# Kernel tuning notes

Hardware: AMD Instinct MI355X
Metric: run time of the kernel (lower is better)

Reference implementation:

```python
import jax, jax.numpy as jnp
import numpy as np

B, S, E, H, D, F = 8, 512, 768, 12, 64, 3072
EPS = 1e-5
SQRT3 = np.float32(np.sqrt(3.0))


def _ln(x, g, b):
    m = jnp.mean(x, -1, keepdims=True)
    v = jnp.mean((x - m) ** 2, -1, keepdims=True)
    return (x - m) * jax.lax.rsqrt(v + EPS) * g + b


def _gelu_new(x):
    return 0.5 * x * (1.0 + jnp.tanh(0.7978845608028654 * (x + 0.044715 * x * x * x)))


def _heads(t):  # [B,T,E] -> [B,T,H,D]
    return t.reshape(t.shape[0], t.shape[1], H, D)


def _self_attn(xl, Wq, Wk, Wv, Wo, bo, mask):
    q = _heads(xl @ Wq)
    k = _heads(xl @ Wk)
    v = _heads(xl @ Wv)
    w = jnp.einsum('bqhd,bkhd->bhqk', q, k) / 8.0  # scale=True, sqrt(64)
    w = jnp.where(mask, -1e9, w)
    p = jax.nn.softmax(w, axis=-1)
    o = jnp.einsum('bhqk,bkhd->bqhd', p, v).reshape(xl.shape)
    present = jnp.stack([k.transpose(0, 2, 1, 3), v.transpose(0, 2, 1, 3)])  # [2,B,H,S,D]
    return o @ Wo + bo, present


def _cross_attn(xl, el, wq, bq, wk, bk, wv, bv, wp, bp, mask):
    q = _heads(xl @ wq + bq)
    k = _heads(el @ wk + bk)
    v = _heads(el @ wv + bv)
    w = jnp.einsum('bqhd,bkhd->bhqk', q, k) / 8.0
    w = jnp.where(mask, -1e4, w)
    p = jax.nn.softmax(w, axis=-1)
    o = jnp.einsum('bhqk,bkhd->bqhd', p, v).reshape(xl.shape)
    return o @ wp + bp  # Conv1D: x @ W + b


def _block(x, encoder_output, mask_queries, mask_sa, mask_enc, tau,
           Wq, Wk, Wv, Wo, bo,
           fcq_w, fcq_b, fck_w, fck_b, fcv_w, fcv_b, cproj_w, cproj_b,
           ln1_g, ln1_b, ln2_g, ln2_b,
           cfc_w, cfc_b, cproj2_w, cproj2_b,
           a1_w, a1_b, a2_w, a2_b, a3_w, a3_b):
    thr = jnp.asarray(tau, jnp.float32)
    sa, present = _self_attn(_ln(x, ln1_g, ln1_b), Wq, Wk, Wv, Wo, bo, mask_sa)
    a = x + sa  # resid dropout = identity (eval)
    al = _ln(a, ln1_g, ln1_b)

    def cross(idx):
        el = _ln(encoder_output[:, idx], ln1_g, ln1_b)
        return _cross_attn(al, el, fcq_w, fcq_b, fck_w, fck_b, fcv_w, fcv_b,
                           cproj_w, cproj_b, mask_enc)

    e1, e2, e3 = cross(0), cross(1), cross(2)

    def gate(e, w, b):
        alpha = jax.nn.sigmoid(jnp.concatenate([a, e], -1) @ w + b)
        lm = jnp.where(alpha > thr, 1.0, 0.0)
        vm = jnp.where(alpha < 1.0 - thr, 1.0, 0.0)
        return alpha * lm * a + (1.0 - alpha) * vm * e

    enc_att = (gate(e1, a1_w, a1_b) + gate(e2, a2_w, a2_b) + gate(e3, a3_w, a3_b)) / SQRT3
    aq = enc_att * mask_queries
    m = _gelu_new(_ln(aq, ln2_g, ln2_b) @ cfc_w + cfc_b) @ cproj2_w + cproj2_b
    out = (aq + m) * mask_queries
    return out, present


def setup_inputs() -> dict:
    key = jax.random.key(0)
    ks = jax.random.split(key, 40)
    p = lambda k, shp: (jax.random.normal(k, shp, jnp.float32) * 0.02)
    x = jax.random.normal(ks[0], (B, S, E), jnp.float32)
    encoder_output = jax.random.normal(ks[1], (B, 3, S, E), jnp.float32)
    mask_queries = jnp.ones((B, S, 1), jnp.float32)
    causal = ~jnp.tril(jnp.ones((S, S), bool))  # True = masked
    mask_self_attention = jnp.broadcast_to(causal[None, None], (B, 1, S, S))
    mask_encoder = jax.random.bernoulli(ks[2], 0.1, (B, 1, 1, S))
    d = dict(x=x, encoder_output=encoder_output, mask_queries=mask_queries,
             mask_self_attention=mask_self_attention, mask_encoder=mask_encoder,
             i=0, tau=0,
             Wq=p(ks[3], (E, E)), Wk=p(ks[4], (E, E)), Wv=p(ks[5], (E, E)),
             Wo=p(ks[6], (E, E)), bo=jnp.zeros((E,), jnp.float32),
             fcq_w=p(ks[7], (E, E)), fcq_b=jnp.zeros((E,), jnp.float32),
             fck_w=p(ks[8], (E, E)), fck_b=jnp.zeros((E,), jnp.float32),
             fcv_w=p(ks[9], (E, E)), fcv_b=jnp.zeros((E,), jnp.float32),
             cproj_w=p(ks[10], (E, E)), cproj_b=jnp.zeros((E,), jnp.float32),
             ln1_g=jnp.ones((E,), jnp.float32), ln1_b=jnp.zeros((E,), jnp.float32),
             ln2_g=jnp.ones((E,), jnp.float32), ln2_b=jnp.zeros((E,), jnp.float32),
             cfc_w=p(ks[11], (E, F)), cfc_b=jnp.zeros((F,), jnp.float32),
             cproj2_w=p(ks[12], (F, E)), cproj2_b=jnp.zeros((E,), jnp.float32),
             a1_w=p(ks[13], (2 * E, E)), a1_b=jnp.zeros((E,), jnp.float32),
             a2_w=p(ks[14], (2 * E, E)), a2_b=jnp.zeros((E,), jnp.float32),
             a3_w=p(ks[15], (2 * E, E)), a3_b=jnp.zeros((E,), jnp.float32))
    return d


def reference(x, encoder_output, mask_queries, mask_self_attention, mask_encoder, i, tau,
              Wq, Wk, Wv, Wo, bo,
              fcq_w, fcq_b, fck_w, fck_b, fcv_w, fcv_b, cproj_w, cproj_b,
              ln1_g, ln1_b, ln2_g, ln2_b,
              cfc_w, cfc_b, cproj2_w, cproj2_b,
              a1_w, a1_b, a2_w, a2_b, a3_w, a3_b):
    return _block(x, encoder_output, mask_queries, mask_self_attention, mask_encoder, tau,
                  Wq, Wk, Wv, Wo, bo,
                  fcq_w, fcq_b, fck_w, fck_b, fcv_w, fcv_b, cproj_w, cproj_b,
                  ln1_g, ln1_b, ln2_g, ln2_b,
                  cfc_w, cfc_b, cproj2_w, cproj2_b,
                  a1_w, a1_b, a2_w, a2_b, a3_w, a3_b)
```

## Files before the change

### kernel.cpp

```cpp
#include <hip/hip_runtime.h>
#include <hip/hip_bf16.h>
#include <math.h>

typedef __hip_bfloat16 bf16;
typedef __attribute__((ext_vector_type(8))) short s16x8;
typedef __attribute__((ext_vector_type(4))) float f32x4;

#define BB 8
#define SS 512
#define EE 768
#define HH 12
#define DD 64
#define FF 3072
#define NTOK (BB * SS)
#define NE ((size_t)NTOK * EE)

#define TM 128
#define TN 128
#define TK 32

#define QT 64
#define KT 64

#define FLAG_RES  4
#define FLAG_GELU 8
#define FLAG_FIN  16
#define FLAG_CBSD 32
#define FLAG_QKV  128
#define FLAG_KV   256
#define FLAG_GSEG 512

#define AS1 const __attribute__((address_space(1))) void*
#define AS3 __attribute__((address_space(3))) void*

__device__ __forceinline__ float gelu_new(float x) {
    float u2 = 1.5957691216057308f * (x + 0.044715f * x * x * x);
    return x / (1.0f + __expf(-u2));
}

__global__ __launch_bounds__(256) void tcast_all_kernel(
    const float* s0, const float* s1, const float* s2, const float* s3,
    const float* s4, const float* s5, const float* s6, const float* s7,
    const float* s8, const float* s9, const float* s10, const float* s11,
    const float* s12,
    bf16* d0, bf16* d1, bf16* d2, bf16* d3, bf16* d4, bf16* d5, bf16* d6,
    bf16* d7, bf16* d8, bf16* d9, bf16* d10, bf16* d11, bf16* d12,
    const float* fckb, const float* fcvb, const float* a0, const float* a1,
    const float* a2, float* kvb, float* gb)
{
    int bid = blockIdx.x;
    int tid = threadIdx.x;
    if (bid >= 12672) {
        int i = (bid - 12672) * 256 + tid;
        int seg = i / 768, off = i % 768;
        if (seg == 0)      kvb[off]       = fckb[off];
        else if (seg == 1) kvb[768 + off] = fcvb[off];
        else if (seg == 2) gb[off]        = a0[off];
        else if (seg == 3) gb[768 + off]  = a1[off];
        else               gb[1536 + off] = a2[off];
        return;
    }
    const int start[14] = {0, 576, 1152, 1728, 2304, 2880, 3456, 4032,
                           4608, 5760, 6912, 8064, 10368, 12672};
    const float* srcs[13] = {s0,s1,s2,s3,s4,s5,s6,s7,s8,s9,s10,s11,s12};
    bf16* dsts[13] = {d0,d1,d2,d3,d4,d5,d6,d7,d8,d9,d10,d11,d12};

    int idx = 0;
    #pragma unroll
    for (int i = 1; i < 13; ++i) if (bid >= start[i]) idx = i;
    int R = (idx < 8) ? 768 : (idx < 11) ? 1536 : (idx == 11) ? 768 : 3072;
    int C = (idx < 8) ? 768 : (idx < 11) ? 768 : (idx == 11) ? 3072 : 768;
    const float* src = srcs[idx];
    bf16* dst = dsts[idx];

    int t = bid - start[idx];
    int gx = C >> 5;
    int c0 = (t % gx) << 5;
    int r0 = (t / gx) << 5;

    __shared__ float tb[32][33];
    int x = tid & 31, y = tid >> 5;
    #pragma unroll
    for (int i = 0; i < 4; ++i) {
        int r = y + i * 8;
        tb[r][x] = src[(size_t)(r0 + r) * C + c0 + x];
    }
    __syncthreads();
    #pragma unroll
    for (int i = 0; i < 4; ++i) {
        int c = y + i * 8;
        dst[(size_t)(c0 + c) * R + r0 + x] = __float2bfloat16(tb[x][c]);
    }
}

__device__ __forceinline__ void ln_body(
    const float* __restrict__ x, bf16* __restrict__ y,
    const float* __restrict__ g, const float* __restrict__ bta, int tid)
{
    float v0 = x[tid], v1 = x[tid + 256], v2 = x[tid + 512];
    float s1 = v0 + v1 + v2;
    float s2 = v0 * v0 + v1 * v1 + v2 * v2;
    #pragma unroll
    for (int o = 32; o > 0; o >>= 1) {
        s1 += __shfl_down(s1, o);
        s2 += __shfl_down(s2, o);
    }
    __shared__ float r1[4], r2[4];
    if ((tid & 63) == 0) { r1[tid >> 6] = s1; r2[tid >> 6] = s2; }
    __syncthreads();
    float mean = (r1[0] + r1[1] + r1[2] + r1[3]) * (1.0f / 768.0f);
    float ssq  = (r2[0] + r2[1] + r2[2] + r2[3]) * (1.0f / 768.0f);
    float rstd = rsqrtf(ssq - mean * mean + 1e-5f);
    y[tid]       = __float2bfloat16((v0 - mean) * rstd * g[tid]       + bta[tid]);
    y[tid + 256] = __float2bfloat16((v1 - mean) * rstd * g[tid + 256] + bta[tid + 256]);
    y[tid + 512] = __float2bfloat16((v2 - mean) * rstd * g[tid + 512] + bta[tid + 512]);
}

__global__ __launch_bounds__(256) void ln_kernel(
    const float* __restrict__ in, bf16* __restrict__ out,
    const float* __restrict__ g, const float* __restrict__ bta)
{
    int row = blockIdx.x;
    ln_body(in + (size_t)row * EE, out + (size_t)row * EE, g, bta, threadIdx.x);
}

__global__ __launch_bounds__(256) void ln_all_kernel(
    const float* __restrict__ x, const float* __restrict__ enc,
    bf16* __restrict__ outx, bf16* __restrict__ outenc,
    const float* __restrict__ g, const float* __restrict__ bta)
{
    int row = blockIdx.x;
    if (row < NTOK) {
        ln_body(x + (size_t)row * EE, outx + (size_t)row * EE, g, bta, threadIdx.x);
    } else {
        int r = row - NTOK;
        int idx = r >> 12, b = (r >> 9) & 7, s = r & 511;
        ln_body(enc + (((size_t)b * 3 + idx) * SS + s) * EE,
                outenc + (size_t)r * EE, g, bta, threadIdx.x);
    }
}

template <int FLAGS>
__device__ __forceinline__ void mgemm_body(
    int bx, int by, bf16* smem,
    const bf16* __restrict__ A, const bf16* __restrict__ A2,
    const bf16* __restrict__ Wt, const float* __restrict__ bias,
    float* __restrict__ Cf, bf16* __restrict__ Cb, bf16* __restrict__ Cb2,
    int ldcb, const float* __restrict__ Rsrc, const float* __restrict__ maskq,
    int Nn, int K, int lda)
{
    constexpr bool f_res  = FLAGS & FLAG_RES;
    constexpr bool f_gelu = FLAGS & FLAG_GELU;
    constexpr bool f_fin  = FLAGS & FLAG_FIN;
    constexpr bool f_cbsd = FLAGS & FLAG_CBSD;
    constexpr bool f_qkv  = FLAGS & FLAG_QKV;
    constexpr bool f_kv   = FLAGS & FLAG_KV;
    constexpr bool f_gseg = FLAGS & FLAG_GSEG;

    const int BUFE = TM * TK + TN * TK;
    int tid = threadIdx.x;
    int w = tid >> 6, l = tid & 63;
    int row0 = bx * TM, col0 = by * TN;

    int wr = (w >> 1) * 64, wc = (w & 1) * 64;
    int lr = l & 15, lg = l >> 4;

    const bf16* Wb = Wt;
    const float* bb_ = bias;
    if constexpr (f_gseg) {
        int seg = row0 >> 12;
        Wb = Wt + (size_t)seg * 1536 * 768;
        bb_ = bias + seg * 768;
    }

    f32x4 acc[4][4];
    #pragma unroll
    for (int m = 0; m < 4; ++m)
        #pragma unroll
        for (int n = 0; n < 4; ++n) acc[m][n] = (f32x4){0.f, 0.f, 0.f, 0.f};

    auto stage = [&](int buf, int kb) {
        bf16* As_ = smem + buf * BUFE;
        bf16* Bs_ = As_ + TM * TK;
        #pragma unroll
        for (int i = 0; i < 2; ++i) {
            int e = (i * 256 + tid) * 8;
            int r = e >> 5;
            int c = (e & 31) ^ ((r & 3) << 3);
            const bf16* asrc;
            if constexpr (f_gseg) {
                int kg = kb + c;
                if (kg < 768) asrc = A  + (size_t)((row0 + r) & 4095) * lda + kg;
                else          asrc = A2 + (size_t)(row0 + r) * lda + (kg - 768);
            } else {
                asrc = A + (size_t)(row0 + r) * lda + kb + c;
            }
            __builtin_amdgcn_global_load_lds((AS1)asrc,
                (AS3)((char*)As_ + i * 4096 + w * 1024), 16, 0, 0);
            __builtin_amdgcn_global_load_lds((AS1)(Wb + (size_t)(col0 + r) * K + kb + c),
                (AS3)((char*)Bs_ + i * 4096 + w * 1024), 16, 0, 0);
        }
    };

    int nk = K / TK;
    stage(0, 0);
    stage(1, TK);
    stage(2, 2 * TK);

    for (int t = 0; t < nk; ++t) {
        int cur = t % 3;
        int ahead = nk - 1 - t; if (ahead > 2) ahead = 2;
        if (ahead == 2)      asm volatile("s_waitcnt vmcnt(8)" ::: "memory");
        else if (ahead == 1) asm volatile("s_waitcnt vmcnt(4)" ::: "memory");
        else                 asm volatile("s_waitcnt vmcnt(0)" ::: "memory");
        __builtin_amdgcn_s_barrier();

        const char* As = (const char*)(smem + cur * BUFE);
        const char* Bs = As + TM * TK * 2;
        s16x8 af[4], bfr[4];
        #pragma unroll
        for (int m = 0; m < 4; ++m) {
            int row = wr + m * 16 + lr;
            af[m] = *(const s16x8*)(As + row * 64 +
                      ((lg * 16) ^ ((row & 3) << 4)));
        }
        #pragma unroll
        for (int n = 0; n < 4; ++n) {
            int row = wc + n * 16 + lr;
            bfr[n] = *(const s16x8*)(Bs + row * 64 +
                      ((lg * 16) ^ ((row & 3) << 4)));
        }
        #pragma unroll
        for (int m = 0; m < 4; ++m)
            #pragma unroll
            for (int n = 0; n < 4; ++n)
                acc[m][n] = __builtin_amdgcn_mfma_f32_16x16x32_bf16(
                    af[m], bfr[n], acc[m][n], 0, 0, 0);

        asm volatile("s_waitcnt lgkmcnt(0)" ::: "memory");
        __builtin_amdgcn_s_barrier();
        if (t + 3 < nk) stage(cur, (t + 3) * TK);
    }

    int gh0 = (col0 + wc) >> 6;

    if constexpr (f_qkv || f_kv || f_cbsd) {
        bool vquad = (f_qkv && gh0 >= 24) || (f_kv && gh0 >= 12);
        bf16* Tb = smem + w * 4096;
        int bb = (row0 + wr) >> 9;
        int s0 = (row0 + wr) & 511;

        #pragma unroll
        for (int m = 0; m < 4; ++m)
            #pragma unroll
            for (int n = 0; n < 4; ++n)
                #pragma unroll
                for (int j = 0; j < 4; ++j) {
                    int col = col0 + wc + n * 16 + lr;
                    float v = acc[m][n][j];
                    if (bb_) v += bb_[col];
                    int rl = m * 16 + lg * 4 + j, cl = n * 16 + lr;
                    if (vquad)
                        *(bf16*)((char*)Tb + cl * 128 + ((rl * 2) ^ ((cl & 7) << 4))) =
                            __float2bfloat16(v);
                    else
                        Tb[rl * 64 + (cl ^ ((rl & 7) << 3))] = __float2bfloat16(v);
                }
        if (vquad) {
            int hV = gh0 - (f_qkv ? 24 : 12);
            bf16* vb = Cb2 + (((size_t)bb * HH + hV) * DD) * SS + s0;
            #pragma unroll
            for (int p = 0; p < 8; ++p) {
                int dl = p * 8 + (l >> 3);
                int ch = l & 7;
                int cs = ch ^ (dl & 7);
                s16x8 vv = *(const s16x8*)((char*)Tb + dl * 128 + cs * 16);
                *(s16x8*)(vb + (size_t)dl * SS + ch * 8) = vv;
            }
            if constexpr (f_qkv) {
                asm volatile("s_waitcnt lgkmcnt(0)" ::: "memory");
                #pragma unroll
                for (int m = 0; m < 4; ++m)
                    #pragma unroll
                    for (int n = 0; n < 4; ++n)
                        #pragma unroll
                        for (int j = 0; j < 4; ++j) {
                            int rl = m * 16 + lg * 4 + j, cl = n * 16 + lr;
                            Tb[rl * 64 + (cl ^ ((rl & 7) << 3))] =
                                __float2bfloat16(acc[m][n][j]);
                        }
                bf16* vbhsd = (bf16*)Cf;
                bf16* dst2 = vbhsd + (((size_t)bb * HH + hV) * SS + s0) * DD;
                #pragma unroll
                for (int p = 0; p < 8; ++p) {
                    int rl = p * 8 + (l >> 3);
                    int c8 = (l & 7) * 8;
                    s16x8 vv = *(const s16x8*)&Tb[rl * 64 + (c8 ^ ((rl & 7) << 3))];
                    *(s16x8*)(dst2 + (size_t)rl * DD + c8) = vv;
                }
            }
        } else {
            bf16* dst;
            if constexpr (f_qkv)
                dst = (gh0 < 12)
                    ? Cb + (((size_t)bb * HH + gh0) * SS + s0) * DD
                    : Cb + NE + (((size_t)bb * HH + (gh0 - 12)) * SS + s0) * DD;
            else
                dst = Cb + (((size_t)bb * HH + gh0) * SS + s0) * DD;
            #pragma unroll
            for (int p = 0; p < 8; ++p) {
                int rl = p * 8 + (l >> 3);
                int c8 = (l & 7) * 8;
                s16x8 vv = *(const s16x8*)&Tb[rl * 64 + (c8 ^ ((rl & 7) << 3))];
                *(s16x8*)(dst + (size_t)rl * DD + c8) = vv;
            }
        }
    } else {
        #pragma unroll
        for (int m = 0; m < 4; ++m) {
            #pragma unroll
            for (int n = 0; n < 4; ++n) {
                #pragma unroll
                for (int j = 0; j < 4; ++j) {
                    int row = row0 + wr + m * 16 + lg * 4 + j;
                    int col = col0 + wc + n * 16 + lr;
                    size_t lin = (size_t)row * Nn + col;
                    float v = acc[m][n][j];
                    if (bb_)                 v += bb_[col];
                    if constexpr (f_res)     v += Rsrc[lin];
                    if constexpr (f_gelu)    v = gelu_new(v);
                    if constexpr (f_fin)     v = (Rsrc[lin] + v) * maskq[row];
                    if (Cf) Cf[lin] = v;
                    if (Cb) Cb[(size_t)row * ldcb + col] = __float2bfloat16(v);
                }
            }
        }
    }
}

template <int FLAGS>
__global__ __launch_bounds__(256) void mgemm_kernel(
    const bf16* __restrict__ A, const bf16* __restrict__ A2,
    const bf16* __restrict__ Wt, const float* __restrict__ bias,
    float* __restrict__ Cf, bf16* __restrict__ Cb, bf16* __restrict__ Cb2,
    int ldcb, const float* __restrict__ Rsrc, const float* __restrict__ maskq,
    int Nn, int K, int lda)
{
    __shared__ __align__(16) bf16 smem[3 * (TM * TK + TN * TK)];
    mgemm_body<FLAGS>(blockIdx.x, blockIdx.y, smem, A, A2, Wt, bias,
                      Cf, Cb, Cb2, ldcb, Rsrc, maskq, Nn, K, lda);
}

__global__ __launch_bounds__(256) void qkvkv_kernel(
    const bf16* __restrict__ lnb, const bf16* __restrict__ lnenc,
    const bf16* __restrict__ WqkvT, const bf16* __restrict__ fckvT,
    const float* __restrict__ kvb,
    bf16* __restrict__ vbhsd, bf16* __restrict__ qbhb, bf16* __restrict__ vbhb,
    bf16* __restrict__ kb_c, bf16* __restrict__ vb_c)
{
    __shared__ __align__(16) bf16 smem[3 * (TM * TK + TN * TK)];
    int bid = blockIdx.x;
    if (bid < 576) {
        mgemm_body<FLAG_QKV>(bid & 31, bid >> 5, smem, lnb, nullptr, WqkvT, nullptr,
                             (float*)vbhsd, qbhb, vbhb, 0, nullptr, nullptr, 2304, 768, 768);
    } else {
        int t = bid - 576;
        mgemm_body<FLAG_KV>(t % 96, t / 96, smem, lnenc, nullptr, fckvT, kvb,
                            nullptr, kb_c, vb_c, 0, nullptr, nullptr, 1536, 768, 768);
    }
}

__device__ __forceinline__ void fattn_body(
    int bh, int qt, bf16* sm,
    const bf16* __restrict__ Qb, const bf16* __restrict__ Kb,
    const bf16* __restrict__ Vb, const int* __restrict__ maskE,
    bf16* __restrict__ Out, int causal)
{
    int bp = bh / HH, h = bh % HH;
    int bq = bp & 7;
    int tid = threadIdx.x;
    int w = tid >> 6, l = tid & 63;
    int lr = l & 15, g = l >> 4;

    bf16* Qs = sm;
    bf16* Ks = sm + 4096;
    bf16* Vs = sm + 8192;
    bf16* Ps = sm + 12288;

    int p0 = w * 1024 + l * 16;
    {
        const char* qg = (const char*)(Qb + (((size_t)bq * HH + h) * SS + qt * QT) * DD);
        #pragma unroll
        for (int i = 0; i < 2; ++i) {
            int p = i * 4096 + p0;
            int row = p >> 7, cb = p & 127;
            int scb = cb ^ ((row & 7) << 4);
            __builtin_amdgcn_global_load_lds((AS1)(qg + row * 128 + scb),
                (AS3)((char*)Qs + i * 4096 + w * 1024), 16, 0, 0);
        }
    }

    float mrun[4], lrun[4];
    f32x4 oacc[4];
    #pragma unroll
    for (int j = 0; j < 4; ++j) { mrun[j] = -3.0e38f; lrun[j] = 0.f; }
    #pragma unroll
    for (int n = 0; n < 4; ++n) oacc[n] = (f32x4){0.f, 0.f, 0.f, 0.f};

    int ntiles = causal ? (qt + 1) : (SS / KT);
    int qrow_base = w * 16;

    for (int kt = 0; kt < ntiles; ++kt) {
        const char* kg = (const char*)(Kb + ((size_t)bh * SS + kt * KT) * DD);
        const char* vg = (const char*)(Vb + (size_t)bh * DD * SS + (size_t)kt * KT);
        #pragma unroll
        for (int i = 0; i < 2; ++i) {
            int p = i * 4096 + p0;
            int row = p >> 7, cb = p & 127;
            int scb = cb ^ ((row & 7) << 4);
            __builtin_amdgcn_global_load_lds((AS1)(kg + row * 128 + scb),
                (AS3)((char*)Ks + i * 4096 + w * 1024), 16, 0, 0);
            __builtin_amdgcn_global_load_lds((AS1)(vg + (size_t)row * (SS * 2) + scb),
                (AS3)((char*)Vs + i * 4096 + w * 1024), 16, 0, 0);
        }
        int km[4];
        if (maskE) {
            #pragma unroll
            for (int n = 0; n < 4; ++n)
                km[n] = maskE[(size_t)bq * SS + kt * KT + n * 16 + lr];
        }
        __syncthreads();

        f32x4 sacc[4];
        #pragma unroll
        for (int n = 0; n < 4; ++n) sacc[n] = (f32x4){0.f, 0.f, 0.f, 0.f};
        #pragma unroll
        for (int ks = 0; ks < 2; ++ks) {
            int qrow = qrow_base + lr;
            s16x8 aq = *(const s16x8*)((const char*)Qs +
                        qrow * 128 + ((ks * 64 + g * 16) ^ ((qrow & 7) << 4)));
            #pragma unroll
            for (int n = 0; n < 4; ++n) {
                int krow = n * 16 + lr;
                s16x8 bk = *(const s16x8*)((const char*)Ks +
                            krow * 128 + ((ks * 64 + g * 16) ^ ((krow & 7) << 4)));
                sacc[n] = __builtin_amdgcn_mfma_f32_16x16x32_bf16(aq, bk, sacc[n], 0, 0, 0);
            }
        }

        #pragma unroll
        for (int n = 0; n < 4; ++n) {
            #pragma unroll
            for (int j = 0; j < 4; ++j) {
                float v = sacc[n][j] * 0.125f;
                if (causal) {
                    if (kt == qt && (n * 16 + lr > qrow_base + 4 * g + j)) v = -3.0e38f;
                } else {
                    if (km[n] != 0) v = -1e4f;
                }
                sacc[n][j] = v;
            }
        }

        float mx[4];
        #pragma unroll
        for (int j = 0; j < 4; ++j)
            mx[j] = fmaxf(fmaxf(sacc[0][j], sacc[1][j]), fmaxf(sacc[2][j], sacc[3][j]));
        #pragma unroll
        for (int msk = 1; msk < 16; msk <<= 1) {
            #pragma unroll
            for (int j = 0; j < 4; ++j) mx[j] = fmaxf(mx[j], __shfl_xor(mx[j], msk));
        }
        float rs[4], psum[4];
        #pragma unroll
        for (int j = 0; j < 4; ++j) {
            float mn = fmaxf(mrun[j], mx[j]);
            rs[j] = __expf(mrun[j] - mn);
            mrun[j] = mn;
            psum[j] = 0.f;
        }
        #pragma unroll
        for (int n = 0; n < 4; ++n) {
            #pragma unroll
            for (int j = 0; j < 4; ++j) {
                float p = __expf(sacc[n][j] - mrun[j]);
                psum[j] += p;
                int prow = qrow_base + 4 * g + j;
                int key = n * 16 + lr;
                *(bf16*)((char*)Ps + prow * 128 + ((2 * key) ^ ((prow & 7) << 4))) =
                    __float2bfloat16(p);
            }
        }
        #pragma unroll
        for (int msk = 1; msk < 16; msk <<= 1) {
            #pragma unroll
            for (int j = 0; j < 4; ++j) psum[j] += __shfl_xor(psum[j], msk);
        }
        #pragma unroll
        for (int j = 0; j < 4; ++j) lrun[j] = lrun[j] * rs[j] + psum[j];
        #pragma unroll
        for (int n = 0; n < 4; ++n) {
            #pragma unroll
            for (int j = 0; j < 4; ++j) oacc[n][j] *= rs[j];
        }

        #pragma unroll
        for (int ks = 0; ks < 2; ++ks) {
            int prow = qrow_base + lr;
            s16x8 ap = *(const s16x8*)((const char*)Ps +
                        prow * 128 + ((ks * 64 + g * 16) ^ ((prow & 7) << 4)));
            #pragma unroll
            for (int n = 0; n < 4; ++n) {
                int vrow = n * 16 + lr;
                s16x8 bv = *(const s16x8*)((const char*)Vs +
                            vrow * 128 + ((ks * 64 + g * 16) ^ ((vrow & 7) << 4)));
                oacc[n] = __builtin_amdgcn_mfma_f32_16x16x32_bf16(ap, bv, oacc[n], 0, 0, 0);
            }
        }
        __syncthreads();
    }

    float inv[4];
    #pragma unroll
    for (int j = 0; j < 4; ++j) inv[j] = 1.0f / lrun[j];
    #pragma unroll
    for (int n = 0; n < 4; ++n) {
        #pragma unroll
        for (int j = 0; j < 4; ++j) {
            int q = qt * QT + qrow_base + 4 * g + j;
            int d = n * 16 + lr;
            Out[((size_t)bp * SS + q) * EE + h * DD + d] =
                __float2bfloat16(oacc[n][j] * inv[j]);
        }
    }
}

__global__ __launch_bounds__(256) void fattn2_kernel(
    const bf16* __restrict__ Qb, const bf16* __restrict__ Kb,
    const bf16* __restrict__ Vb, const int* __restrict__ maskE,
    bf16* __restrict__ Out, int causal)
{
    __shared__ __align__(16) bf16 sm[4 * 4096];
    fattn_body(blockIdx.x, blockIdx.y, sm, Qb, Kb, Vb, maskE, Out, causal);
}

__global__ __launch_bounds__(256) void fattn_self_cast_kernel(
    const bf16* __restrict__ Qb, const bf16* __restrict__ Kb,
    const bf16* __restrict__ Vb, bf16* __restrict__ Out,
    const bf16* __restrict__ kb, const bf16* __restrict__ vb,
    float* __restrict__ kp, float* __restrict__ vp)
{
    __shared__ __align__(16) bf16 sm[4 * 4096];
    int bid = blockIdx.x;
    if (bid < 768) {
        fattn_body(bid % 96, bid / 96, sm, Qb, Kb, Vb, nullptr, Out, 1);
    } else {
        size_t i = ((size_t)(bid - 768) * 256 + threadIdx.x) * 8;
        s16x8 kv = *(const s16x8*)(kb + i);
        s16x8 vv = *(const s16x8*)(vb + i);
        #pragma unroll
        for (int j = 0; j < 8; ++j) {
            unsigned int bk = ((unsigned int)(unsigned short)kv[j]) << 16;
            unsigned int bv = ((unsigned int)(unsigned short)vv[j]) << 16;
            kp[i + j] = __uint_as_float(bk);
            vp[i + j] = __uint_as_float(bv);
        }
    }
}

__global__ __launch_bounds__(256) void gate3ln_kernel(
    const bf16* __restrict__ logits, const float* __restrict__ a,
    const bf16* __restrict__ e, float* __restrict__ acc, bf16* __restrict__ lnout,
    const int* __restrict__ tau, const float* __restrict__ maskq,
    const float* __restrict__ g, const float* __restrict__ bta)
{
    int row = blockIdx.x;
    int tid = threadIdx.x;
    float thr = (float)tau[0];
    float mq = maskq[row] * 0.57735026918962576f;
    size_t base = (size_t)row * EE;

    float aq[3];
    float s1 = 0.f, s2 = 0.f;
    #pragma unroll
    for (int c = 0; c < 3; ++c) {
        size_t i = base + tid + c * 256;
        float av = a[i];
        float r = 0.f;
        #pragma unroll
        for (int idx = 0; idx < 3; ++idx) {
            float lg = __bfloat162float(logits[(size_t)idx * NE + i]);
            float ev = __bfloat162float(e[(size_t)idx * NE + i]);
            float al = 1.0f / (1.0f + __expf(-lg));
            float lm = (al > thr) ? 1.0f : 0.0f;
            float vm = (al < 1.0f - thr) ? 1.0f : 0.0f;
            r += al * lm * av + (1.0f - al) * vm * ev;
        }
        float v = r * mq;
        acc[i] = v;
        aq[c] = v;
        s1 += v;
        s2 += v * v;
    }
    #pragma unroll
    for (int o = 32; o > 0; o >>= 1) {
        s1 += __shfl_down(s1, o);
        s2 += __shfl_down(s2, o);
    }
    __shared__ float r1[4], r2[4];
    if ((tid & 63) == 0) { r1[tid >> 6] = s1; r2[tid >> 6] = s2; }
    __syncthreads();
    float mean = (r1[0] + r1[1] + r1[2] + r1[3]) * (1.0f / 768.0f);
    float ssq  = (r2[0] + r2[1] + r2[2] + r2[3]) * (1.0f / 768.0f);
    float rstd = rsqrtf(ssq - mean * mean + 1e-5f);

    bf16* y = lnout + base;
    #pragma unroll
    for (int c = 0; c < 3; ++c) {
        int col = tid + c * 256;
        y[col] = __float2bfloat16((aq[c] - mean) * rstd * g[col] + bta[col]);
    }
}

extern "C" void kernel_launch(void* const* d_in, const int* in_sizes, int n_in,
                              void* d_out, int out_size, void* d_ws, size_t ws_size,
                              hipStream_t stream)
{
    const float* x        = (const float*)d_in[0];
    const float* enc      = (const float*)d_in[1];
    const float* maskq    = (const float*)d_in[2];
    const int*   mask_enc = (const int*)d_in[4];
    const int*   tau      = (const int*)d_in[6];
    const float* Wq = (const float*)d_in[7];
    const float* Wk = (const float*)d_in[8];
    const float* Wv = (const float*)d_in[9];
    const float* Wo = (const float*)d_in[10];
    const float* bo = (const float*)d_in[11];
    const float* fcq_w = (const float*)d_in[12];
    const float* fcq_b = (const float*)d_in[13];
    const float* fck_w = (const float*)d_in[14];
    const float* fck_b = (const float*)d_in[15];
    const float* fcv_w = (const float*)d_in[16];
    const float* fcv_b = (const float*)d_in[17];
    const float* cproj_w = (const float*)d_in[18];
    const float* cproj_b = (const float*)d_in[19];
    const float* ln1_g = (const float*)d_in[20];
    const float* ln1_b = (const float*)d_in[21];
    const float* ln2_g = (const float*)d_in[22];
    const float* ln2_b = (const float*)d_in[23];
    const float* cfc_w = (const float*)d_in[24];
    const float* cfc_b = (const float*)d_in[25];
    const float* cproj2_w = (const float*)d_in[26];
    const float* cproj2_b = (const float*)d_in[27];
    const float* aw[3] = {(const float*)d_in[28], (const float*)d_in[30], (const float*)d_in[32]};
    const float* ab[3] = {(const float*)d_in[29], (const float*)d_in[31], (const float*)d_in[33]};

    float* out   = (float*)d_out;
    float* kpres = out + NE;
    float* vpres = out + 2 * NE;

    float* ws  = (float*)d_ws;
    float* a     = ws;
    float* acc   = ws + NE;
    float* R     = ws + 2 * NE;
    bf16*  kb_c    = (bf16*)R;
    bf16*  vb_c    = kb_c + 3 * NE;
    bf16*  logitsb = (bf16*)R;
    bf16*  mlphb   = (bf16*)R;

    bf16* bbase = (bf16*)(ws + 5 * NE);
    bf16* lnb   = bbase;
    bf16* atts  = bbase;
    bf16* lnenc = bbase + NE;
    bf16* attc  = lnenc;
    bf16* a_bf  = bbase + 4 * NE;
    bf16* e_bf  = bbase + 5 * NE;
    bf16* qbhb  = bbase + 8 * NE;
    bf16* kbhb  = bbase + 9 * NE;
    bf16* vbhb  = bbase + 10 * NE;
    bf16* vbhsd = bbase + 11 * NE;
    bf16* wp    = bbase + 12 * NE;
    bf16* WqkvT = wp;          wp += 3 * 768 * 768;
    bf16* WoT = wp;            wp += 768 * 768;
    bf16* fcqT = wp;           wp += 768 * 768;
    bf16* fckvT = wp;          wp += 2 * 768 * 768;
    bf16* cprojT = wp;         wp += 768 * 768;
    bf16* awT = wp;            wp += (size_t)3 * 1536 * 768;
    bf16* cfcT = wp;           wp += (size_t)768 * 3072;
    bf16* cproj2T = wp;        wp += (size_t)3072 * 768;
    float* kvb = (float*)wp;
    float* gb  = kvb + 1536;

    dim3 blk(256);

    tcast_all_kernel<<<12687, blk, 0, stream>>>(
        Wq, Wk, Wv, Wo, fcq_w, fck_w, fcv_w, cproj_w,
        aw[0], aw[1], aw[2], cfc_w, cproj2_w,
        WqkvT, WqkvT + 768 * 768, WqkvT + 2 * 768 * 768, WoT, fcqT,
        fckvT, fckvT + 768 * 768, cprojT,
        awT, awT + 1536 * 768, awT + 2 * 1536 * 768, cfcT, cproj2T,
        fck_b, fcv_b, ab[0], ab[1], ab[2], kvb, gb);
    ln_all_kernel<<<4 * NTOK, blk, 0, stream>>>(x, enc, lnb, lnenc, ln1_g, ln1_b);
    qkvkv_kernel<<<1728, blk, 0, stream>>>(lnb, lnenc, WqkvT, fckvT, kvb,
        vbhsd, qbhb, vbhb, kb_c, vb_c);
    fattn_self_cast_kernel<<<768 + 1536, blk, 0, stream>>>(
        qbhb, kbhb, vbhb, atts, kbhb, vbhsd, kpres, vpres);
    mgemm_kernel<FLAG_RES><<<dim3(32, 6), blk, 0, stream>>>(atts, nullptr, WoT, bo,
        a, a_bf, nullptr, 768, x, nullptr, 768, 768, 768);
    ln_kernel<<<NTOK, blk, 0, stream>>>(a, lnb, ln1_g, ln1_b);
    mgemm_kernel<FLAG_CBSD><<<dim3(32, 6), blk, 0, stream>>>(lnb, nullptr, fcqT, fcq_b,
        nullptr, qbhb, nullptr, 0, nullptr, nullptr, 768, 768, 768);
    fattn2_kernel<<<dim3(288, 8), blk, 0, stream>>>(qbhb, kb_c, vb_c, mask_enc, attc, 0);
    mgemm_kernel<0><<<dim3(96, 6), blk, 0, stream>>>(attc, nullptr, cprojT, cproj_b,
        nullptr, e_bf, nullptr, 768, nullptr, nullptr, 768, 768, 768);
    mgemm_kernel<FLAG_GSEG><<<dim3(96, 6), blk, 0, stream>>>(a_bf, e_bf, awT, gb,
        nullptr, logitsb, nullptr, 768, nullptr, nullptr, 768, 1536, 768);
    gate3ln_kernel<<<NTOK, blk, 0, stream>>>(logitsb, a, e_bf, acc, lnb,
        tau, maskq, ln2_g, ln2_b);
    mgemm_kernel<FLAG_GELU><<<dim3(32, 24), blk, 0, stream>>>(lnb, nullptr, cfcT, cfc_b,
        nullptr, mlphb, nullptr, 3072, nullptr, nullptr, 3072, 768, 768);
    mgemm_kernel<FLAG_FIN><<<dim3(32, 6), blk, 0, stream>>>(mlphb, nullptr, cproj2T, cproj2_b,
        out, nullptr, nullptr, 0, acc, maskq, 768, 3072, 3072);
}
```

Measured before the change: 544.2 us.

## Move cross-attention KV GEMM into the self-attention kernel with interleaved block roles

The encoder K/V projection GEMM is split out of the QKV launch and merged into the causal self-attention plus present-cast kernel. Block IDs are interleaved in groups of nine (2 attention, 3 GEMM, 4 cast blocks) so the different workloads run side by side. The goal is to fill the GPU better, since the QKV GEMM alone is a small grid and the causal attention blocks have uneven durations. In exchange, the fused kernel now reserves the larger GEMM shared-memory footprint for every block, which may lower occupancy for the attention and cast blocks.

New measurement: 554.9 us. No clear change (+2.0%).

```diff
diff --git a/kernel.cpp b/kernel.cpp
--- a/kernel.cpp
+++ b/kernel.cpp
@@ -351,23 +351,14 @@
                       Cf, Cb, Cb2, ldcb, Rsrc, maskq, Nn, K, lda);
 }
 
-__global__ __launch_bounds__(256) void qkvkv_kernel(
-    const bf16* __restrict__ lnb, const bf16* __restrict__ lnenc,
-    const bf16* __restrict__ WqkvT, const bf16* __restrict__ fckvT,
-    const float* __restrict__ kvb,
-    bf16* __restrict__ vbhsd, bf16* __restrict__ qbhb, bf16* __restrict__ vbhb,
-    bf16* __restrict__ kb_c, bf16* __restrict__ vb_c)
+__global__ __launch_bounds__(256) void qkv_kernel(
+    const bf16* __restrict__ lnb, const bf16* __restrict__ WqkvT,
+    bf16* __restrict__ vbhsd, bf16* __restrict__ qbhb, bf16* __restrict__ vbhb)
 {
     __shared__ __align__(16) bf16 smem[3 * (TM * TK + TN * TK)];
-    int bid = blockIdx.x;
-    if (bid < 576) {
-        mgemm_body<FLAG_QKV>(bid & 31, bid >> 5, smem, lnb, nullptr, WqkvT, nullptr,
-                             (float*)vbhsd, qbhb, vbhb, 0, nullptr, nullptr, 2304, 768, 768);
-    } else {
-        int t = bid - 576;
-        mgemm_body<FLAG_KV>(t % 96, t / 96, smem, lnenc, nullptr, fckvT, kvb,
-                            nullptr, kb_c, vb_c, 0, nullptr, nullptr, 1536, 768, 768);
-    }
+    mgemm_body<FLAG_QKV>(blockIdx.x & 31, blockIdx.x >> 5, smem, lnb, nullptr,
+                         WqkvT, nullptr, (float*)vbhsd, qbhb, vbhb, 0,
+                         nullptr, nullptr, 2304, 768, 768);
 }
 
 __device__ __forceinline__ void fattn_body(
@@ -544,20 +535,30 @@
     fattn_body(blockIdx.x, blockIdx.y, sm, Qb, Kb, Vb, maskE, Out, causal);
 }
 
-__global__ __launch_bounds__(256) void fattn_self_cast_kernel(
+__global__ __launch_bounds__(256) void fattn_kvcast_kernel(
     const bf16* __restrict__ Qb, const bf16* __restrict__ Kb,
     const bf16* __restrict__ Vb, bf16* __restrict__ Out,
-    const bf16* __restrict__ kb, const bf16* __restrict__ vb,
+    const bf16* __restrict__ lnenc, const bf16* __restrict__ fckvT,
+    const float* __restrict__ kvb,
+    bf16* __restrict__ kb_c, bf16* __restrict__ vb_c,
+    const bf16* __restrict__ kb, const bf16* __restrict__ vbs,
     float* __restrict__ kp, float* __restrict__ vp)
 {
-    __shared__ __align__(16) bf16 sm[4 * 4096];
+    __shared__ __align__(16) bf16 smem[3 * (TM * TK + TN * TK)];
     int bid = blockIdx.x;
-    if (bid < 768) {
-        fattn_body(bid % 96, bid / 96, sm, Qb, Kb, Vb, nullptr, Out, 1);
+    int g9 = bid / 9, r9 = bid % 9;
+    if (r9 < 2) {
+        int f = g9 * 2 + r9;
+        fattn_body(f % 96, f / 96, smem, Qb, Kb, Vb, nullptr, Out, 1);
+    } else if (r9 < 5) {
+        int t = g9 * 3 + (r9 - 2);
+        mgemm_body<FLAG_KV>(t % 96, t / 96, smem, lnenc, nullptr, fckvT, kvb,
+                            nullptr, kb_c, vb_c, 0, nullptr, nullptr, 1536, 768, 768);
     } else {
-        size_t i = ((size_t)(bid - 768) * 256 + threadIdx.x) * 8;
+        int c = g9 * 4 + (r9 - 5);
+        size_t i = ((size_t)c * 256 + threadIdx.x) * 8;
         s16x8 kv = *(const s16x8*)(kb + i);
-        s16x8 vv = *(const s16x8*)(vb + i);
+        s16x8 vv = *(const s16x8*)(vbs + i);
         #pragma unroll
         for (int j = 0; j < 8; ++j) {
             unsigned int bk = ((unsigned int)(unsigned short)kv[j]) << 16;
@@ -701,10 +702,9 @@
         awT, awT + 1536 * 768, awT + 2 * 1536 * 768, cfcT, cproj2T,
         fck_b, fcv_b, ab[0], ab[1], ab[2], kvb, gb);
     ln_all_kernel<<<4 * NTOK, blk, 0, stream>>>(x, enc, lnb, lnenc, ln1_g, ln1_b);
-    qkvkv_kernel<<<1728, blk, 0, stream>>>(lnb, lnenc, WqkvT, fckvT, kvb,
-        vbhsd, qbhb, vbhb, kb_c, vb_c);
-    fattn_self_cast_kernel<<<768 + 1536, blk, 0, stream>>>(
-        qbhb, kbhb, vbhb, atts, kbhb, vbhsd, kpres, vpres);
+    qkv_kernel<<<576, blk, 0, stream>>>(lnb, WqkvT, vbhsd, qbhb, vbhb);
+    fattn_kvcast_kernel<<<3456, blk, 0, stream>>>(qbhb, kbhb, vbhb, atts,
+        lnenc, fckvT, kvb, kb_c, vb_c, kbhb, vbhsd, kpres, vpres);
     mgemm_kernel<FLAG_RES><<<dim3(32, 6), blk, 0, stream>>>(atts, nullptr, WoT, bo,
         a, a_bf, nullptr, 768, x, nullptr, 768, 768, 768);
     ln_kernel<<<NTOK, blk, 0, stream>>>(a, lnb, ln1_g, ln1_b);
```
